# Performance work log

Hardware: AMD Instinct MI355X
Metric: run time of the kernel (lower is better)

## Reference

```python
import jax, jax.numpy as jnp
import numpy as np

N = 100000      # nodes
E = 3200000     # edges
D_IN, D_H, D_OUT = 128, 64, 32


def _lin(key, fan_in, fan_out):
    kw, kb = jax.random.split(key)
    s = 1.0 / np.sqrt(fan_in)
    W = jax.random.uniform(kw, (fan_in, fan_out), jnp.float32, -s, s)
    b = jax.random.uniform(kb, (fan_out,), jnp.float32, -s, s)
    return W, b


def setup_inputs() -> dict:
    key = jax.random.key(0)
    ks = jax.random.split(key, 8)
    x = jax.random.normal(ks[0], (N, D_IN), jnp.float32)
    edge_index = jax.random.randint(ks[1], (2, E), 0, N, dtype=jnp.int32).astype(jnp.int64)
    W1, b1 = _lin(ks[2], D_IN, D_H)      # GCNConv(128, 64)
    W2, b2 = _lin(ks[3], D_H, D_OUT)     # GCNConv(64, 32)
    rW1, rb1 = _lin(ks[4], D_OUT, D_H)   # reconstruction MLP
    rW2, rb2 = _lin(ks[5], D_H, D_IN)
    sW1, sb1 = _lin(ks[6], D_OUT, D_H // 2)  # anomaly scorer MLP
    sW2, sb2 = _lin(ks[7], D_H // 2, 1)
    return {"x": x, "edge_index": edge_index,
            "W1": W1, "b1": b1, "W2": W2, "b2": b2,
            "rW1": rW1, "rb1": rb1, "rW2": rW2, "rb2": rb2,
            "sW1": sW1, "sb1": sb1, "sW2": sW2, "sb2": sb2}


def gcn_conv(h, W, b, src, dst, deg_inv_sqrt):
    # GCNConv with added self-loops and symmetric normalization.
    hw = h @ W                                   # [N, out]
    norm = deg_inv_sqrt[src] * deg_inv_sqrt[dst] # [E]
    agg = jax.ops.segment_sum(hw[src] * norm[:, None], dst, num_segments=N)
    agg = agg + hw * (deg_inv_sqrt * deg_inv_sqrt)[:, None]  # self-loop term
    return agg + b


def reference(x, edge_index, W1, b1, W2, b2, rW1, rb1, rW2, rb2, sW1, sb1, sW2, sb2):
    src, dst = edge_index[0], edge_index[1]
    # degree with self-loops (in-degree on target, as in PyG gcn_norm)
    deg = jnp.zeros((N,), x.dtype).at[dst].add(1.0) + 1.0
    dis = jax.lax.rsqrt(deg)
    h = gcn_conv(x, W1, b1, src, dst, dis)
    h = jax.nn.relu(h)                           # relu+dropout(eval=no-op) between convs
    h = gcn_conv(h, W2, b2, src, dst, dis)       # [N, 32]
    x_rec = jax.nn.relu(h @ rW1 + rb1) @ rW2 + rb2           # [N, 128]
    score = jax.nn.sigmoid(jax.nn.relu(h @ sW1 + sb1) @ sW2 + sb2)  # [N, 1]
    return h, x_rec, score
```

## Files before the change

kernel.cpp:

```cpp
#include <hip/hip_runtime.h>
#include <hip/hip_bf16.h>
#include <math.h>


__global__ __launch_bounds__(256) void k_binhist(const void* __restrict__ ei,
                                                 int E, int CS, int B, int shift,
                                                 int ndet,
                                                 int* __restrict__ hist, int C) {
  __shared__ int lh[256];
  __shared__ int s32;
  int t = threadIdx.x;
  if (t == 0) s32 = 0;
  for (int i = t; i < B; i += 256) lh[i] = 0;
  __syncthreads();
  {
    const unsigned* w = (const unsigned*)ei;
    int local = 0;
    for (int i = t; i < ndet; i += 256) local |= (w[2 * i + 1] != 0u);
    if (local) atomicOr(&s32, 1);
  }
  __syncthreads();
  bool is64 = (s32 == 0);
  int c = blockIdx.x;
  int e0 = c * CS, e1 = min(E, e0 + CS);
  for (int e = e0 + t; e < e1; e += 256) {
    int d = is64 ? (int)((const long long*)ei)[(long)E + e]
                 : ((const int*)ei)[(long)E + e];
    atomicAdd(&lh[d >> shift], 1);
  }
  __syncthreads();
  for (int b = t; b < B; b += 256) hist[(long)b * C + c] = lh[b];
}

__global__ __launch_bounds__(256) void k_binscatter(const void* __restrict__ ei,
                                                    int E, int CS, int B, int shift,
                                                    int SB, int ndet,
                                                    const int* __restrict__ scan,
                                                    int C, unsigned* __restrict__ pairs) {
  __shared__ int cur[256];
  __shared__ int s32;
  int t = threadIdx.x;
  if (t == 0) s32 = 0;
  int c = blockIdx.x;
  for (int b = t; b < B; b += 256) cur[b] = scan[(long)b * C + c];
  __syncthreads();
  {
    const unsigned* w = (const unsigned*)ei;
    int local = 0;
    for (int i = t; i < ndet; i += 256) local |= (w[2 * i + 1] != 0u);
    if (local) atomicOr(&s32, 1);
  }
  __syncthreads();
  bool is64 = (s32 == 0);
  int e0 = c * CS, e1 = min(E, e0 + CS);
  unsigned spb1 = (1u << shift) - 1u;
  for (int e = e0 + t; e < e1; e += 256) {
    int s, d;
    if (is64) {
      const long long* p = (const long long*)ei;
      s = (int)p[e]; d = (int)p[(long)E + e];
    } else {
      const int* p = (const int*)ei;
      s = p[e]; d = p[(long)E + e];
    }
    int pos = atomicAdd(&cur[d >> shift], 1);
    pairs[pos] = (((unsigned)d & spb1) << SB) | (unsigned)s;
  }
}

#define BB_CAP 16896
__global__ __launch_bounds__(256) void k_bucketbuild(const unsigned* __restrict__ pairs,
                                                     const int* __restrict__ scan,
                                                     int C, int shift, int SB, int N,
                                                     int* __restrict__ cnt,
                                                     float* __restrict__ dis,
                                                     int* __restrict__ rs,
                                                     int* __restrict__ csr) {
  __shared__ unsigned buf[BB_CAP];
  __shared__ unsigned buf2[BB_CAP];
  __shared__ int h[1024];
  __shared__ int sm[256];
  __shared__ int sh[512];
  int bin = blockIdx.x;
  int base = bin << shift;
  int nn = min(N - base, 1 << shift);
  int t = threadIdx.x;
  unsigned smask = (1u << SB) - 1u;
  int p0 = scan[(long)bin * C];
  int p1 = scan[(long)(bin + 1) * C];
  int ne = p1 - p0;
  bool srt = (ne <= BB_CAP);

  if (srt)
    for (int i = t; i < ne; i += 256) buf[i] = pairs[p0 + i];
  for (int i = t; i < 1024; i += 256) h[i] = 0;
  __syncthreads();

  for (int i = t; i < ne; i += 256)
    atomicAdd(&h[(srt ? buf[i] : pairs[p0 + i]) >> SB], 1);
  __syncthreads();

  int v0 = h[4 * t], v1 = h[4 * t + 1], v2 = h[4 * t + 2], v3 = h[4 * t + 3];
  int s = v0 + v1 + v2 + v3;
  sm[t] = s;
  __syncthreads();
  for (int off = 1; off < 256; off <<= 1) {
    int x = (t >= off) ? sm[t - off] : 0;
    __syncthreads();
    sm[t] += x;
    __syncthreads();
  }
  int run = p0 + sm[t] - s;
  int r0 = run, r1 = run + v0, r2 = r1 + v1, r3 = r2 + v2;
  h[4 * t] = r0; h[4 * t + 1] = r1; h[4 * t + 2] = r2; h[4 * t + 3] = r3;
  if (4 * t + 0 < nn) { cnt[base + 4*t+0] = v0; dis[base + 4*t+0] = rsqrtf((float)v0 + 1.f); rs[base + 4*t+0] = r0; }
  if (4 * t + 1 < nn) { cnt[base + 4*t+1] = v1; dis[base + 4*t+1] = rsqrtf((float)v1 + 1.f); rs[base + 4*t+1] = r1; }
  if (4 * t + 2 < nn) { cnt[base + 4*t+2] = v2; dis[base + 4*t+2] = rsqrtf((float)v2 + 1.f); rs[base + 4*t+2] = r2; }
  if (4 * t + 3 < nn) { cnt[base + 4*t+3] = v3; dis[base + 4*t+3] = rsqrtf((float)v3 + 1.f); rs[base + 4*t+3] = r3; }
  __syncthreads();

  if (srt) {
    for (int i = t; i < 512; i += 256) sh[i] = 0;
    __syncthreads();
    for (int i = t; i < ne; i += 256)
      atomicAdd(&sh[(buf[i] & smask) >> 8], 1);
    __syncthreads();
    int a0 = sh[2 * t], a1 = sh[2 * t + 1];
    int ss = a0 + a1;
    sm[t] = ss;
    __syncthreads();
    for (int off = 1; off < 256; off <<= 1) {
      int x = (t >= off) ? sm[t - off] : 0;
      __syncthreads();
      sm[t] += x;
      __syncthreads();
    }
    int rn = sm[t] - ss;
    sh[2 * t] = rn; sh[2 * t + 1] = rn + a0;
    __syncthreads();
    for (int i = t; i < ne; i += 256) {
      unsigned p = buf[i];
      int pos = atomicAdd(&sh[(p & smask) >> 8], 1);
      buf2[pos] = p;
    }
    __syncthreads();
    for (int i = t; i < ne; i += 256) {
      unsigned p = buf2[i];
      int pos = atomicAdd(&h[p >> SB], 1);
      csr[pos] = (int)(p & smask);
    }
  } else {
    for (int i = p0 + t; i < p1; i += 256) {
      unsigned p = pairs[i];
      int pos = atomicAdd(&h[p >> SB], 1);
      csr[pos] = (int)(p & smask);
    }
  }
}

__global__ __launch_bounds__(1024) void k_scan1(const int* __restrict__ cnt,
                                                int* __restrict__ bsums, int n) {
  __shared__ int sm[1024];
  int t = threadIdx.x;
  long i = (long)blockIdx.x * 1024 + t;
  sm[t] = (i < n) ? cnt[i] : 0;
  __syncthreads();
  for (int s = 512; s > 0; s >>= 1) {
    if (t < s) sm[t] += sm[t + s];
    __syncthreads();
  }
  if (t == 0) bsums[blockIdx.x] = sm[0];
}

__global__ void k_scan2(int* __restrict__ bsums, int nb) {
  __shared__ int sm[128];
  int t = threadIdx.x;
  int v = (t < nb) ? bsums[t] : 0;
  sm[t] = v;
  __syncthreads();
  for (int off = 1; off < 128; off <<= 1) {
    int x = (t >= off) ? sm[t - off] : 0;
    __syncthreads();
    sm[t] += x;
    __syncthreads();
  }
  if (t < nb) bsums[t] = sm[t] - v;
}

__global__ __launch_bounds__(1024) void k_scan3s(const int* __restrict__ in,
                                                 const int* __restrict__ bsums,
                                                 int* __restrict__ out, int n,
                                                 int sentinel) {
  __shared__ int sm[1024];
  int t = threadIdx.x;
  long i = (long)blockIdx.x * 1024 + t;
  int v = (i < n) ? in[i] : 0;
  sm[t] = v;
  __syncthreads();
  for (int off = 1; off < 1024; off <<= 1) {
    int x = (t >= off) ? sm[t - off] : 0;
    __syncthreads();
    sm[t] += x;
    __syncthreads();
  }
  int excl = sm[t] - v + bsums[blockIdx.x];
  if (i < n) out[i] = excl;
  if (sentinel && i == n - 1) out[n] = excl + v;
}

__device__ __forceinline__ float bfu(unsigned short u) {
  return __uint_as_float((unsigned)u << 16);
}
__device__ __forceinline__ float bf_lo(unsigned u) {
  return __uint_as_float(u << 16);
}
__device__ __forceinline__ float bf_hi(unsigned u) {
  return __uint_as_float(u & 0xffff0000u);
}
__device__ __forceinline__ unsigned pack_bf2(float lo, float hi) {
  __hip_bfloat16 a = __float2bfloat16(lo), b = __float2bfloat16(hi);
  return (unsigned)*(unsigned short*)&a | ((unsigned)*(unsigned short*)&b << 16);
}

template <int K, int M, bool BIAS, int ACT, bool ABF16, bool OBF16>
__global__ __launch_bounds__(256) void k_gemm(const void* __restrict__ Av,
                                              const float* __restrict__ W,
                                              const float* __restrict__ bias,
                                              void* __restrict__ Cout, int nrows) {
  constexpr int CP = 4;
  constexpr int TPR = M / CP;
  constexpr int RG = 256 / TPR;
  constexpr int RP = 4;
  constexpr int RT = RG * RP;
  __shared__ __align__(16) float sW[K * M];
  __shared__ __align__(16) float sB[BIAS ? M : 4];

  for (int i = threadIdx.x; i < K * M / 4; i += 256)
    ((float4*)sW)[i] = ((const float4*)W)[i];
  if (BIAS)
    for (int i = threadIdx.x; i < M; i += 256) sB[i] = bias[i];
  __syncthreads();

  const int cg = threadIdx.x % TPR;
  const int rg = threadIdx.x / TPR;
  const long row0 = (long)blockIdx.x * RT + rg;

  const float4* Apf[RP];
  const ushort4* Apb[RP];
  bool valid[RP];
#pragma unroll
  for (int r = 0; r < RP; ++r) {
    long row = row0 + (long)r * RG;
    valid[r] = (row < nrows);
    long rr = valid[r] ? row : 0;
    if (ABF16) Apb[r] = (const ushort4*)((const unsigned short*)Av + rr * K);
    else       Apf[r] = (const float4*)((const float*)Av + rr * K);
  }

  auto loadA = [&](int r, int k4) -> float4 {
    if (!valid[r]) return make_float4(0.f, 0.f, 0.f, 0.f);
    if (ABF16) {
      ushort4 q = Apb[r][k4];
      return make_float4(bfu(q.x), bfu(q.y), bfu(q.z), bfu(q.w));
    }
    return Apf[r][k4];
  };

  float acc[RP][CP] = {};
  float4 a[RP];
#pragma unroll
  for (int r = 0; r < RP; ++r) a[r] = loadA(r, 0);

#pragma unroll 1
  for (int k0 = 0; k0 < K - 4; k0 += 4) {
    float4 an[RP];
#pragma unroll
    for (int r = 0; r < RP; ++r) an[r] = loadA(r, k0 / 4 + 1);
#pragma unroll
    for (int j = 0; j < 4; ++j) {
      float4 w = ((const float4*)(sW + (k0 + j) * M))[cg];
#pragma unroll
      for (int r = 0; r < RP; ++r) {
        float av = (j == 0) ? a[r].x : (j == 1) ? a[r].y : (j == 2) ? a[r].z : a[r].w;
        acc[r][0] += av * w.x;
        acc[r][1] += av * w.y;
        acc[r][2] += av * w.z;
        acc[r][3] += av * w.w;
      }
    }
#pragma unroll
    for (int r = 0; r < RP; ++r) a[r] = an[r];
  }
  {
    const int k0 = K - 4;
#pragma unroll
    for (int j = 0; j < 4; ++j) {
      float4 w = ((const float4*)(sW + (k0 + j) * M))[cg];
#pragma unroll
      for (int r = 0; r < RP; ++r) {
        float av = (j == 0) ? a[r].x : (j == 1) ? a[r].y : (j == 2) ? a[r].z : a[r].w;
        acc[r][0] += av * w.x;
        acc[r][1] += av * w.y;
        acc[r][2] += av * w.z;
        acc[r][3] += av * w.w;
      }
    }
  }

#pragma unroll
  for (int r = 0; r < RP; ++r) {
    long row = row0 + (long)r * RG;
    if (row >= nrows) continue;
    float4 o = make_float4(acc[r][0], acc[r][1], acc[r][2], acc[r][3]);
    if (BIAS) {
      float4 bb = ((const float4*)sB)[cg];
      o.x += bb.x; o.y += bb.y; o.z += bb.z; o.w += bb.w;
    }
    if (ACT == 1) {
      o.x = fmaxf(o.x, 0.f); o.y = fmaxf(o.y, 0.f);
      o.z = fmaxf(o.z, 0.f); o.w = fmaxf(o.w, 0.f);
    }
    if (OBF16) {
      uint2 pk;
      pk.x = pack_bf2(o.x, o.y);
      pk.y = pack_bf2(o.z, o.w);
      ((uint2*)((__hip_bfloat16*)Cout + row * M))[cg] = pk;
    } else {
      ((float4*)((float*)Cout + row * M))[cg] = o;
    }
  }
}

__global__ __launch_bounds__(256) void k_agg64g(const uint2* __restrict__ hw,
                                                const int* __restrict__ csr,
                                                const int* __restrict__ rs,
                                                const int* __restrict__ cnt,
                                                const float* __restrict__ dis,
                                                const float* __restrict__ b,
                                                const float* __restrict__ W2,
                                                unsigned* __restrict__ hw2,
                                                int n) {
  __shared__ __align__(16) float sW2[64 * 32];
  __shared__ __align__(16) float sH[16][68];
  int t = threadIdx.x;
  for (int i = t; i < 64 * 32 / 4; i += 256)
    ((float4*)sW2)[i] = ((const float4*)W2)[i];

  unsigned nd = t >> 4;
  unsigned node = blockIdx.x * 16u + nd;
  unsigned f4 = t & 15;
  bool ok = (node < (unsigned)n);
  float o0 = 0.f, o1 = 0.f, o2 = 0.f, o3 = 0.f;
  if (ok) {
    float dsn = dis[node];
    uint2 su = hw[node * 16u + f4];
    float d2 = dsn * dsn;
    float a0 = bf_lo(su.x) * d2, a1 = bf_hi(su.x) * d2;
    float a2 = bf_lo(su.y) * d2, a3 = bf_hi(su.y) * d2;
    int start = rs[node], deg = cnt[node];
    int e = 0;
    for (; e + 7 < deg; e += 8) {
      unsigned s0 = (unsigned)csr[start + e];
      unsigned s1 = (unsigned)csr[start + e + 1];
      unsigned s2 = (unsigned)csr[start + e + 2];
      unsigned s3 = (unsigned)csr[start + e + 3];
      unsigned s4 = (unsigned)csr[start + e + 4];
      unsigned s5 = (unsigned)csr[start + e + 5];
      unsigned s6 = (unsigned)csr[start + e + 6];
      unsigned s7 = (unsigned)csr[start + e + 7];
      float w0 = dis[s0] * dsn, w1 = dis[s1] * dsn;
      float w2 = dis[s2] * dsn, w3 = dis[s3] * dsn;
      float w4 = dis[s4] * dsn, w5 = dis[s5] * dsn;
      float w6 = dis[s6] * dsn, w7 = dis[s7] * dsn;
      uint2 u0 = hw[s0 * 16u + f4];
      uint2 u1 = hw[s1 * 16u + f4];
      uint2 u2 = hw[s2 * 16u + f4];
      uint2 u3 = hw[s3 * 16u + f4];
      uint2 u4 = hw[s4 * 16u + f4];
      uint2 u5 = hw[s5 * 16u + f4];
      uint2 u6 = hw[s6 * 16u + f4];
      uint2 u7 = hw[s7 * 16u + f4];
      a0 += bf_lo(u0.x) * w0 + bf_lo(u1.x) * w1 + bf_lo(u2.x) * w2 + bf_lo(u3.x) * w3
          + bf_lo(u4.x) * w4 + bf_lo(u5.x) * w5 + bf_lo(u6.x) * w6 + bf_lo(u7.x) * w7;
      a1 += bf_hi(u0.x) * w0 + bf_hi(u1.x) * w1 + bf_hi(u2.x) * w2 + bf_hi(u3.x) * w3
          + bf_hi(u4.x) * w4 + bf_hi(u5.x) * w5 + bf_hi(u6.x) * w6 + bf_hi(u7.x) * w7;
      a2 += bf_lo(u0.y) * w0 + bf_lo(u1.y) * w1 + bf_lo(u2.y) * w2 + bf_lo(u3.y) * w3
          + bf_lo(u4.y) * w4 + bf_lo(u5.y) * w5 + bf_lo(u6.y) * w6 + bf_lo(u7.y) * w7;
      a3 += bf_hi(u0.y) * w0 + bf_hi(u1.y) * w1 + bf_hi(u2.y) * w2 + bf_hi(u3.y) * w3
          + bf_hi(u4.y) * w4 + bf_hi(u5.y) * w5 + bf_hi(u6.y) * w6 + bf_hi(u7.y) * w7;
    }
    for (; e < deg; ++e) {
      unsigned s0 = (unsigned)csr[start + e];
      float w0 = dis[s0] * dsn;
      uint2 u0 = hw[s0 * 16u + f4];
      a0 += bf_lo(u0.x) * w0;
      a1 += bf_hi(u0.x) * w0;
      a2 += bf_lo(u0.y) * w0;
      a3 += bf_hi(u0.y) * w0;
    }
    float4 bb = ((const float4*)b)[f4];
    o0 = fmaxf(a0 + bb.x, 0.f);
    o1 = fmaxf(a1 + bb.y, 0.f);
    o2 = fmaxf(a2 + bb.z, 0.f);
    o3 = fmaxf(a3 + bb.w, 0.f);
  }
  ((float4*)&sH[nd][4 * f4])[0] = make_float4(o0, o1, o2, o3);
  __syncthreads();
  if (ok) {
    float acc0 = 0.f, acc1 = 0.f;
#pragma unroll 8
    for (int k = 0; k < 64; ++k) {
      float hv = sH[nd][k];
      float2 w = *(const float2*)(sW2 + k * 32 + 2 * f4);
      acc0 += hv * w.x;
      acc1 += hv * w.y;
    }
    hw2[node * 16u + f4] = pack_bf2(acc0, acc1);
  }
}

__global__ __launch_bounds__(256) void k_agg32p(const uint2* __restrict__ hw,
                                                const int* __restrict__ csr,
                                                const int* __restrict__ rs,
                                                const int* __restrict__ cnt,
                                                const float* __restrict__ dis,
                                                const float* __restrict__ b,
                                                float* __restrict__ out, int n) {
  unsigned node = blockIdx.x * 32u + (threadIdx.x >> 3);
  if (node >= (unsigned)n) return;
  unsigned f4 = threadIdx.x & 7;
  float dsn = dis[node];
  uint2 su = hw[node * 8u + f4];
  float d2 = dsn * dsn;
  float a0 = bf_lo(su.x) * d2, a1 = bf_hi(su.x) * d2;
  float a2 = bf_lo(su.y) * d2, a3 = bf_hi(su.y) * d2;
  int start = rs[node], deg = cnt[node];
  int e = 0;
  for (; e + 7 < deg; e += 8) {
    unsigned s0 = (unsigned)csr[start + e];
    unsigned s1 = (unsigned)csr[start + e + 1];
    unsigned s2 = (unsigned)csr[start + e + 2];
    unsigned s3 = (unsigned)csr[start + e + 3];
    unsigned s4 = (unsigned)csr[start + e + 4];
    unsigned s5 = (unsigned)csr[start + e + 5];
    unsigned s6 = (unsigned)csr[start + e + 6];
    unsigned s7 = (unsigned)csr[start + e + 7];
    float w0 = dis[s0] * dsn, w1 = dis[s1] * dsn;
    float w2 = dis[s2] * dsn, w3 = dis[s3] * dsn;
    float w4 = dis[s4] * dsn, w5 = dis[s5] * dsn;
    float w6 = dis[s6] * dsn, w7 = dis[s7] * dsn;
    uint2 u0 = hw[s0 * 8u + f4];
    uint2 u1 = hw[s1 * 8u + f4];
    uint2 u2 = hw[s2 * 8u + f4];
    uint2 u3 = hw[s3 * 8u + f4];
    uint2 u4 = hw[s4 * 8u + f4];
    uint2 u5 = hw[s5 * 8u + f4];
    uint2 u6 = hw[s6 * 8u + f4];
    uint2 u7 = hw[s7 * 8u + f4];
    a0 += bf_lo(u0.x) * w0 + bf_lo(u1.x) * w1 + bf_lo(u2.x) * w2 + bf_lo(u3.x) * w3
        + bf_lo(u4.x) * w4 + bf_lo(u5.x) * w5 + bf_lo(u6.x) * w6 + bf_lo(u7.x) * w7;
    a1 += bf_hi(u0.x) * w0 + bf_hi(u1.x) * w1 + bf_hi(u2.x) * w2 + bf_hi(u3.x) * w3
        + bf_hi(u4.x) * w4 + bf_hi(u5.x) * w5 + bf_hi(u6.x) * w6 + bf_hi(u7.x) * w7;
    a2 += bf_lo(u0.y) * w0 + bf_lo(u1.y) * w1 + bf_lo(u2.y) * w2 + bf_lo(u3.y) * w3
        + bf_lo(u4.y) * w4 + bf_lo(u5.y) * w5 + bf_lo(u6.y) * w6 + bf_lo(u7.y) * w7;
    a3 += bf_hi(u0.y) * w0 + bf_hi(u1.y) * w1 + bf_hi(u2.y) * w2 + bf_hi(u3.y) * w3
        + bf_hi(u4.y) * w4 + bf_hi(u5.y) * w5 + bf_hi(u6.y) * w6 + bf_hi(u7.y) * w7;
  }
  for (; e < deg; ++e) {
    unsigned s0 = (unsigned)csr[start + e];
    float w0 = dis[s0] * dsn;
    uint2 u0 = hw[s0 * 8u + f4];
    a0 += bf_lo(u0.x) * w0;
    a1 += bf_hi(u0.x) * w0;
    a2 += bf_lo(u0.y) * w0;
    a3 += bf_hi(u0.y) * w0;
  }
  float4 bb = ((const float4*)b)[f4];
  ((float4*)(out + node * 32u))[f4] =
      make_float4(a0 + bb.x, a1 + bb.y, a2 + bb.z, a3 + bb.w);
}

__global__ __launch_bounds__(256) void k_tail(const float* __restrict__ h,
                                              const float* __restrict__ rW1,
                                              const float* __restrict__ rb1,
                                              const float* __restrict__ rW2,
                                              const float* __restrict__ rb2,
                                              const float* __restrict__ sW1,
                                              const float* __restrict__ sb1,
                                              const float* __restrict__ sW2,
                                              const float* __restrict__ sb2,
                                              float* __restrict__ x_rec,
                                              float* __restrict__ score, int n) {
  __shared__ __align__(16) float sRW1[32 * 64];
  __shared__ __align__(16) float sRW2[64 * 128];
  __shared__ __align__(16) float sSW1[32 * 32];
  __shared__ __align__(16) float sRB1[64];
  __shared__ __align__(16) float sRB2[128];
  __shared__ __align__(16) float sSB1[32];
  __shared__ __align__(16) float sSW2[32];
  __shared__ float sH[64 * 33];
  __shared__ float sT[64 * 65];
  __shared__ float sS[64 * 33];
  int t = threadIdx.x;
  for (int i = t; i < 32 * 64 / 4; i += 256) ((float4*)sRW1)[i] = ((const float4*)rW1)[i];
  for (int i = t; i < 64 * 128 / 4; i += 256) ((float4*)sRW2)[i] = ((const float4*)rW2)[i];
  for (int i = t; i < 32 * 32 / 4; i += 256) ((float4*)sSW1)[i] = ((const float4*)sW1)[i];
  if (t < 64) sRB1[t] = rb1[t];
  else if (t < 192) sRB2[t - 64] = rb2[t - 64];
  else if (t < 224) sSB1[t - 192] = sb1[t - 192];
  else sSW2[t - 224] = sW2[t - 224];

  long base = (long)blockIdx.x * 64;
  int nn = (int)min(64L, (long)n - base);
  if (nn < 0) nn = 0;
  for (int i = t; i < 64 * 8; i += 256) {
    int node = i >> 3, q = i & 7;
    float4 v = (node < nn) ? ((const float4*)(h + (base + node) * 32))[q]
                           : make_float4(0.f, 0.f, 0.f, 0.f);
    sH[node * 33 + 4 * q]     = v.x;
    sH[node * 33 + 4 * q + 1] = v.y;
    sH[node * 33 + 4 * q + 2] = v.z;
    sH[node * 33 + 4 * q + 3] = v.w;
  }
  __syncthreads();

  {
    int cg = t & 15, rg = t >> 4;
    float acc[4][4] = {};
    for (int k = 0; k < 32; ++k) {
      float4 w = ((const float4*)(sRW1 + k * 64))[cg];
      float a0 = sH[rg * 33 + k];
      float a1 = sH[(rg + 16) * 33 + k];
      float a2 = sH[(rg + 32) * 33 + k];
      float a3 = sH[(rg + 48) * 33 + k];
      acc[0][0] += a0 * w.x; acc[0][1] += a0 * w.y; acc[0][2] += a0 * w.z; acc[0][3] += a0 * w.w;
      acc[1][0] += a1 * w.x; acc[1][1] += a1 * w.y; acc[1][2] += a1 * w.z; acc[1][3] += a1 * w.w;
      acc[2][0] += a2 * w.x; acc[2][1] += a2 * w.y; acc[2][2] += a2 * w.z; acc[2][3] += a2 * w.w;
      acc[3][0] += a3 * w.x; acc[3][1] += a3 * w.y; acc[3][2] += a3 * w.z; acc[3][3] += a3 * w.w;
    }
    float4 bb = ((const float4*)sRB1)[cg];
#pragma unroll
    for (int m = 0; m < 4; ++m) {
      int row = rg + 16 * m;
      sT[row * 65 + 4 * cg]     = fmaxf(acc[m][0] + bb.x, 0.f);
      sT[row * 65 + 4 * cg + 1] = fmaxf(acc[m][1] + bb.y, 0.f);
      sT[row * 65 + 4 * cg + 2] = fmaxf(acc[m][2] + bb.z, 0.f);
      sT[row * 65 + 4 * cg + 3] = fmaxf(acc[m][3] + bb.w, 0.f);
    }
  }
  {
    int cg = t & 7, rg = t >> 3;
    float acc[2][4] = {};
    for (int k = 0; k < 32; ++k) {
      float4 w = ((const float4*)(sSW1 + k * 32))[cg];
      float a0 = sH[rg * 33 + k];
      float a1 = sH[(rg + 32) * 33 + k];
      acc[0][0] += a0 * w.x; acc[0][1] += a0 * w.y; acc[0][2] += a0 * w.z; acc[0][3] += a0 * w.w;
      acc[1][0] += a1 * w.x; acc[1][1] += a1 * w.y; acc[1][2] += a1 * w.z; acc[1][3] += a1 * w.w;
    }
    float4 bb = ((const float4*)sSB1)[cg];
#pragma unroll
    for (int m = 0; m < 2; ++m) {
      int row = rg + 32 * m;
      sS[row * 33 + 4 * cg]     = fmaxf(acc[m][0] + bb.x, 0.f);
      sS[row * 33 + 4 * cg + 1] = fmaxf(acc[m][1] + bb.y, 0.f);
      sS[row * 33 + 4 * cg + 2] = fmaxf(acc[m][2] + bb.z, 0.f);
      sS[row * 33 + 4 * cg + 3] = fmaxf(acc[m][3] + bb.w, 0.f);
    }
  }
  __syncthreads();

  {
    int cg = t & 31, rg = t >> 5;
    float acc[8][4] = {};
    for (int k = 0; k < 64; ++k) {
      float4 w = ((const float4*)(sRW2 + k * 128))[cg];
#pragma unroll
      for (int m = 0; m < 8; ++m) {
        float a = sT[(rg + 8 * m) * 65 + k];
        acc[m][0] += a * w.x; acc[m][1] += a * w.y;
        acc[m][2] += a * w.z; acc[m][3] += a * w.w;
      }
    }
    float4 bb = ((const float4*)sRB2)[cg];
#pragma unroll
    for (int m = 0; m < 8; ++m) {
      int row = rg + 8 * m;
      if (row < nn) {
        float4 o = make_float4(acc[m][0] + bb.x, acc[m][1] + bb.y,
                               acc[m][2] + bb.z, acc[m][3] + bb.w);
        ((float4*)(x_rec + (base + row) * 128))[cg] = o;
      }
    }
  }
  if (t < nn) {
    float acc = 0.f;
    for (int j = 0; j < 32; ++j) acc += sS[t * 33 + j] * sSW2[j];
    score[base + t] = 1.0f / (1.0f + expf(-(acc + sb2[0])));
  }
}

extern "C" void kernel_launch(void* const* d_in, const int* in_sizes, int n_in,
                              void* d_out, int out_size, void* d_ws, size_t ws_size,
                              hipStream_t stream) {
  const float* x   = (const float*)d_in[0];
  const void*  ei  = d_in[1];
  const float* W1  = (const float*)d_in[2];
  const float* b1  = (const float*)d_in[3];
  const float* W2  = (const float*)d_in[4];
  const float* b2  = (const float*)d_in[5];
  const float* rW1 = (const float*)d_in[6];
  const float* rb1 = (const float*)d_in[7];
  const float* rW2 = (const float*)d_in[8];
  const float* rb2 = (const float*)d_in[9];
  const float* sW1 = (const float*)d_in[10];
  const float* sb1 = (const float*)d_in[11];
  const float* sW2 = (const float*)d_in[12];
  const float* sb2 = (const float*)d_in[13];

  const int N = in_sizes[0] / 128;
  const int E = in_sizes[1] / 2;
  const int ndet = E < 4096 ? E : 4096;

  int shift = 9;
  while ((((long)N + (1L << shift) - 1) >> shift) > 256) ++shift;
  const int SB = 32 - shift;
  const int B = (int)(((long)N + (1L << shift) - 1) >> shift);
  const int C = 512;
  const int CS = (E + C - 1) / C;
  const int L = B * C;

  char* w = (char*)d_ws;
  auto alloc = [&](size_t bytes) {
    char* p = w;
    w += (bytes + 255) & ~(size_t)255;
    return p;
  };
  int*   cnt    = (int*)alloc((size_t)N * 4);
  int*   rs     = (int*)alloc((size_t)N * 4);
  float* dis    = (float*)alloc((size_t)N * 4);
  int*   bsumsL = (int*)alloc(1024);
  int*   bscan  = (int*)alloc(((size_t)L + 1) * 4);
  int*   csr    = (int*)alloc((size_t)E * 4);
  unsigned* pairs = (unsigned*)alloc((size_t)E * 4);
  uint2* hw1 = (uint2*)alloc((size_t)N * 64 * 2);
  unsigned* hw2 = (unsigned*)alloc((size_t)N * 32 * 2);

  float* h_out = (float*)d_out;
  float* x_rec = h_out + (long)N * 32;
  float* score = x_rec + (long)N * 128;

  k_binhist<<<C, 256, 0, stream>>>(ei, E, CS, B, shift, ndet, bscan, C);
  int nbL = (L + 1023) / 1024;
  k_scan1<<<nbL, 1024, 0, stream>>>(bscan, bsumsL, L);
  k_scan2<<<1, 128, 0, stream>>>(bsumsL, nbL);
  k_scan3s<<<nbL, 1024, 0, stream>>>(bscan, bsumsL, bscan, L, 1);
  k_binscatter<<<C, 256, 0, stream>>>(ei, E, CS, B, shift, SB, ndet, bscan, C, pairs);
  k_bucketbuild<<<B, 256, 0, stream>>>(pairs, bscan, C, shift, SB, N, cnt, dis, rs, csr);

  k_gemm<128, 64, false, 0, false, true><<<(N + 63) / 64, 256, 0, stream>>>(x, W1, nullptr, hw1, N);
  k_agg64g<<<(N + 15) / 16, 256, 0, stream>>>(hw1, csr, rs, cnt, dis, b1, W2, hw2, N);

  k_agg32p<<<(N + 31) / 32, 256, 0, stream>>>((const uint2*)hw2, csr, rs, cnt, dis, b2, h_out, N);

  k_tail<<<(N + 63) / 64, 256, 0, stream>>>(h_out, rW1, rb1, rW2, rb2,
                                            sW1, sb1, sW2, sb2, x_rec, score, N);
}
```

Before: 281.1 us.

## Fuse second-layer aggregation with reconstruction and scorer MLP tail

Merges the layer-2 aggregation kernel and the MLP tail kernel into one kernel. Each block aggregates 32 nodes, keeps the resulting h in shared memory and runs both MLPs on it directly, so h is no longer re-read from global memory and one launch is removed. The 32KB shared copy of rW2 is dropped and that weight is read straight from global/L1, shrinking shared memory per block. In exchange every block reloads the tail weights for only 32 nodes, and the MLP phase waits on the slowest node's gather in each block.

Result: faster. 264.4 us, median of 2 (-5.9%).

```diff
diff --git a/kernel.cpp b/kernel.cpp
--- a/kernel.cpp
+++ b/kernel.cpp
@@ -419,128 +419,119 @@
   }
 }
 
-__global__ __launch_bounds__(256) void k_agg32p(const uint2* __restrict__ hw,
-                                                const int* __restrict__ csr,
-                                                const int* __restrict__ rs,
-                                                const int* __restrict__ cnt,
-                                                const float* __restrict__ dis,
-                                                const float* __restrict__ b,
-                                                float* __restrict__ out, int n) {
-  unsigned node = blockIdx.x * 32u + (threadIdx.x >> 3);
-  if (node >= (unsigned)n) return;
-  unsigned f4 = threadIdx.x & 7;
-  float dsn = dis[node];
-  uint2 su = hw[node * 8u + f4];
-  float d2 = dsn * dsn;
-  float a0 = bf_lo(su.x) * d2, a1 = bf_hi(su.x) * d2;
-  float a2 = bf_lo(su.y) * d2, a3 = bf_hi(su.y) * d2;
-  int start = rs[node], deg = cnt[node];
-  int e = 0;
-  for (; e + 7 < deg; e += 8) {
-    unsigned s0 = (unsigned)csr[start + e];
-    unsigned s1 = (unsigned)csr[start + e + 1];
-    unsigned s2 = (unsigned)csr[start + e + 2];
-    unsigned s3 = (unsigned)csr[start + e + 3];
-    unsigned s4 = (unsigned)csr[start + e + 4];
-    unsigned s5 = (unsigned)csr[start + e + 5];
-    unsigned s6 = (unsigned)csr[start + e + 6];
-    unsigned s7 = (unsigned)csr[start + e + 7];
-    float w0 = dis[s0] * dsn, w1 = dis[s1] * dsn;
-    float w2 = dis[s2] * dsn, w3 = dis[s3] * dsn;
-    float w4 = dis[s4] * dsn, w5 = dis[s5] * dsn;
-    float w6 = dis[s6] * dsn, w7 = dis[s7] * dsn;
-    uint2 u0 = hw[s0 * 8u + f4];
-    uint2 u1 = hw[s1 * 8u + f4];
-    uint2 u2 = hw[s2 * 8u + f4];
-    uint2 u3 = hw[s3 * 8u + f4];
-    uint2 u4 = hw[s4 * 8u + f4];
-    uint2 u5 = hw[s5 * 8u + f4];
-    uint2 u6 = hw[s6 * 8u + f4];
-    uint2 u7 = hw[s7 * 8u + f4];
-    a0 += bf_lo(u0.x) * w0 + bf_lo(u1.x) * w1 + bf_lo(u2.x) * w2 + bf_lo(u3.x) * w3
-        + bf_lo(u4.x) * w4 + bf_lo(u5.x) * w5 + bf_lo(u6.x) * w6 + bf_lo(u7.x) * w7;
-    a1 += bf_hi(u0.x) * w0 + bf_hi(u1.x) * w1 + bf_hi(u2.x) * w2 + bf_hi(u3.x) * w3
-        + bf_hi(u4.x) * w4 + bf_hi(u5.x) * w5 + bf_hi(u6.x) * w6 + bf_hi(u7.x) * w7;
-    a2 += bf_lo(u0.y) * w0 + bf_lo(u1.y) * w1 + bf_lo(u2.y) * w2 + bf_lo(u3.y) * w3
-        + bf_lo(u4.y) * w4 + bf_lo(u5.y) * w5 + bf_lo(u6.y) * w6 + bf_lo(u7.y) * w7;
-    a3 += bf_hi(u0.y) * w0 + bf_hi(u1.y) * w1 + bf_hi(u2.y) * w2 + bf_hi(u3.y) * w3
-        + bf_hi(u4.y) * w4 + bf_hi(u5.y) * w5 + bf_hi(u6.y) * w6 + bf_hi(u7.y) * w7;
-  }
-  for (; e < deg; ++e) {
-    unsigned s0 = (unsigned)csr[start + e];
-    float w0 = dis[s0] * dsn;
-    uint2 u0 = hw[s0 * 8u + f4];
-    a0 += bf_lo(u0.x) * w0;
-    a1 += bf_hi(u0.x) * w0;
-    a2 += bf_lo(u0.y) * w0;
-    a3 += bf_hi(u0.y) * w0;
-  }
-  float4 bb = ((const float4*)b)[f4];
-  ((float4*)(out + node * 32u))[f4] =
-      make_float4(a0 + bb.x, a1 + bb.y, a2 + bb.z, a3 + bb.w);
-}
-
-__global__ __launch_bounds__(256) void k_tail(const float* __restrict__ h,
-                                              const float* __restrict__ rW1,
-                                              const float* __restrict__ rb1,
-                                              const float* __restrict__ rW2,
-                                              const float* __restrict__ rb2,
-                                              const float* __restrict__ sW1,
-                                              const float* __restrict__ sb1,
-                                              const float* __restrict__ sW2,
-                                              const float* __restrict__ sb2,
-                                              float* __restrict__ x_rec,
-                                              float* __restrict__ score, int n) {
+__global__ __launch_bounds__(256) void k_aggtail(const uint2* __restrict__ hw,
+                                                 const int* __restrict__ csr,
+                                                 const int* __restrict__ rs,
+                                                 const int* __restrict__ cnt,
+                                                 const float* __restrict__ dis,
+                                                 const float* __restrict__ b2,
+                                                 const float* __restrict__ rW1,
+                                                 const float* __restrict__ rb1,
+                                                 const float* __restrict__ rW2,
+                                                 const float* __restrict__ rb2,
+                                                 const float* __restrict__ sW1,
+                                                 const float* __restrict__ sb1,
+                                                 const float* __restrict__ sW2,
+                                                 const float* __restrict__ sb2,
+                                                 float* __restrict__ h_out,
+                                                 float* __restrict__ x_rec,
+                                                 float* __restrict__ score, int n) {
   __shared__ __align__(16) float sRW1[32 * 64];
-  __shared__ __align__(16) float sRW2[64 * 128];
   __shared__ __align__(16) float sSW1[32 * 32];
   __shared__ __align__(16) float sRB1[64];
   __shared__ __align__(16) float sRB2[128];
   __shared__ __align__(16) float sSB1[32];
   __shared__ __align__(16) float sSW2[32];
-  __shared__ float sH[64 * 33];
-  __shared__ float sT[64 * 65];
-  __shared__ float sS[64 * 33];
+  __shared__ float sH[32 * 33];
+  __shared__ float sT[32 * 65];
+  __shared__ float sS[32 * 33];
   int t = threadIdx.x;
   for (int i = t; i < 32 * 64 / 4; i += 256) ((float4*)sRW1)[i] = ((const float4*)rW1)[i];
-  for (int i = t; i < 64 * 128 / 4; i += 256) ((float4*)sRW2)[i] = ((const float4*)rW2)[i];
   for (int i = t; i < 32 * 32 / 4; i += 256) ((float4*)sSW1)[i] = ((const float4*)sW1)[i];
   if (t < 64) sRB1[t] = rb1[t];
   else if (t < 192) sRB2[t - 64] = rb2[t - 64];
   else if (t < 224) sSB1[t - 192] = sb1[t - 192];
   else sSW2[t - 224] = sW2[t - 224];
 
-  long base = (long)blockIdx.x * 64;
-  int nn = (int)min(64L, (long)n - base);
+  unsigned ndl = t >> 3;
+  unsigned node = blockIdx.x * 32u + ndl;
+  unsigned f4 = t & 7;
+  bool ok = (node < (unsigned)n);
+  float o0 = 0.f, o1 = 0.f, o2 = 0.f, o3 = 0.f;
+  if (ok) {
+    float dsn = dis[node];
+    uint2 su = hw[node * 8u + f4];
+    float d2 = dsn * dsn;
+    float a0 = bf_lo(su.x) * d2, a1 = bf_hi(su.x) * d2;
+    float a2 = bf_lo(su.y) * d2, a3 = bf_hi(su.y) * d2;
+    int start = rs[node], deg = cnt[node];
+    int e = 0;
+    for (; e + 7 < deg; e += 8) {
+      unsigned s0 = (unsigned)csr[start + e];
+      unsigned s1 = (unsigned)csr[start + e + 1];
+      unsigned s2 = (unsigned)csr[start + e + 2];
+      unsigned s3 = (unsigned)csr[start + e + 3];
+      unsigned s4 = (unsigned)csr[start + e + 4];
+      unsigned s5 = (unsigned)csr[start + e + 5];
+      unsigned s6 = (unsigned)csr[start + e + 6];
+      unsigned s7 = (unsigned)csr[start + e + 7];
+      float w0 = dis[s0] * dsn, w1 = dis[s1] * dsn;
+      float w2 = dis[s2] * dsn, w3 = dis[s3] * dsn;
+      float w4 = dis[s4] * dsn, w5 = dis[s5] * dsn;
+      float w6 = dis[s6] * dsn, w7 = dis[s7] * dsn;
+      uint2 u0 = hw[s0 * 8u + f4];
+      uint2 u1 = hw[s1 * 8u + f4];
+      uint2 u2 = hw[s2 * 8u + f4];
+      uint2 u3 = hw[s3 * 8u + f4];
+      uint2 u4 = hw[s4 * 8u + f4];
+      uint2 u5 = hw[s5 * 8u + f4];
+      uint2 u6 = hw[s6 * 8u + f4];
+      uint2 u7 = hw[s7 * 8u + f4];
+      a0 += bf_lo(u0.x) * w0 + bf_lo(u1.x) * w1 + bf_lo(u2.x) * w2 + bf_lo(u3.x) * w3
+          + bf_lo(u4.x) * w4 + bf_lo(u5.x) * w5 + bf_lo(u6.x) * w6 + bf_lo(u7.x) * w7;
+      a1 += bf_hi(u0.x) * w0 + bf_hi(u1.x) * w1 + bf_hi(u2.x) * w2 + bf_hi(u3.x) * w3
+          + bf_hi(u4.x) * w4 + bf_hi(u5.x) * w5 + bf_hi(u6.x) * w6 + bf_hi(u7.x) * w7;
+      a2 += bf_lo(u0.y) * w0 + bf_lo(u1.y) * w1 + bf_lo(u2.y) * w2 + bf_lo(u3.y) * w3
+          + bf_lo(u4.y) * w4 + bf_lo(u5.y) * w5 + bf_lo(u6.y) * w6 + bf_lo(u7.y) * w7;
+      a3 += bf_hi(u0.y) * w0 + bf_hi(u1.y) * w1 + bf_hi(u2.y) * w2 + bf_hi(u3.y) * w3
+          + bf_hi(u4.y) * w4 + bf_hi(u5.y) * w5 + bf_hi(u6.y) * w6 + bf_hi(u7.y) * w7;
+    }
+    for (; e < deg; ++e) {
+      unsigned s0 = (unsigned)csr[start + e];
+      float w0 = dis[s0] * dsn;
+      uint2 u0 = hw[s0 * 8u + f4];
+      a0 += bf_lo(u0.x) * w0;
+      a1 += bf_hi(u0.x) * w0;
+      a2 += bf_lo(u0.y) * w0;
+      a3 += bf_hi(u0.y) * w0;
+    }
+    float4 bb = ((const float4*)b2)[f4];
+    o0 = a0 + bb.x; o1 = a1 + bb.y; o2 = a2 + bb.z; o3 = a3 + bb.w;
+    ((float4*)(h_out + node * 32u))[f4] = make_float4(o0, o1, o2, o3);
+  }
+  sH[ndl * 33 + 4 * f4]     = o0;
+  sH[ndl * 33 + 4 * f4 + 1] = o1;
+  sH[ndl * 33 + 4 * f4 + 2] = o2;
+  sH[ndl * 33 + 4 * f4 + 3] = o3;
+  __syncthreads();
+
+  long base = (long)blockIdx.x * 32;
+  int nn = (int)min(32L, (long)n - base);
   if (nn < 0) nn = 0;
-  for (int i = t; i < 64 * 8; i += 256) {
-    int node = i >> 3, q = i & 7;
-    float4 v = (node < nn) ? ((const float4*)(h + (base + node) * 32))[q]
-                           : make_float4(0.f, 0.f, 0.f, 0.f);
-    sH[node * 33 + 4 * q]     = v.x;
-    sH[node * 33 + 4 * q + 1] = v.y;
-    sH[node * 33 + 4 * q + 2] = v.z;
-    sH[node * 33 + 4 * q + 3] = v.w;
-  }
-  __syncthreads();
 
   {
     int cg = t & 15, rg = t >> 4;
-    float acc[4][4] = {};
+    float acc[2][4] = {};
     for (int k = 0; k < 32; ++k) {
       float4 w = ((const float4*)(sRW1 + k * 64))[cg];
       float a0 = sH[rg * 33 + k];
       float a1 = sH[(rg + 16) * 33 + k];
-      float a2 = sH[(rg + 32) * 33 + k];
-      float a3 = sH[(rg + 48) * 33 + k];
       acc[0][0] += a0 * w.x; acc[0][1] += a0 * w.y; acc[0][2] += a0 * w.z; acc[0][3] += a0 * w.w;
       acc[1][0] += a1 * w.x; acc[1][1] += a1 * w.y; acc[1][2] += a1 * w.z; acc[1][3] += a1 * w.w;
-      acc[2][0] += a2 * w.x; acc[2][1] += a2 * w.y; acc[2][2] += a2 * w.z; acc[2][3] += a2 * w.w;
-      acc[3][0] += a3 * w.x; acc[3][1] += a3 * w.y; acc[3][2] += a3 * w.z; acc[3][3] += a3 * w.w;
     }
     float4 bb = ((const float4*)sRB1)[cg];
 #pragma unroll
-    for (int m = 0; m < 4; ++m) {
+    for (int m = 0; m < 2; ++m) {
       int row = rg + 16 * m;
       sT[row * 65 + 4 * cg]     = fmaxf(acc[m][0] + bb.x, 0.f);
       sT[row * 65 + 4 * cg + 1] = fmaxf(acc[m][1] + bb.y, 0.f);
@@ -550,33 +541,27 @@
   }
   {
     int cg = t & 7, rg = t >> 3;
-    float acc[2][4] = {};
+    float acc[4] = {};
     for (int k = 0; k < 32; ++k) {
       float4 w = ((const float4*)(sSW1 + k * 32))[cg];
       float a0 = sH[rg * 33 + k];
-      float a1 = sH[(rg + 32) * 33 + k];
-      acc[0][0] += a0 * w.x; acc[0][1] += a0 * w.y; acc[0][2] += a0 * w.z; acc[0][3] += a0 * w.w;
-      acc[1][0] += a1 * w.x; acc[1][1] += a1 * w.y; acc[1][2] += a1 * w.z; acc[1][3] += a1 * w.w;
+      acc[0] += a0 * w.x; acc[1] += a0 * w.y; acc[2] += a0 * w.z; acc[3] += a0 * w.w;
     }
     float4 bb = ((const float4*)sSB1)[cg];
-#pragma unroll
-    for (int m = 0; m < 2; ++m) {
-      int row = rg + 32 * m;
-      sS[row * 33 + 4 * cg]     = fmaxf(acc[m][0] + bb.x, 0.f);
-      sS[row * 33 + 4 * cg + 1] = fmaxf(acc[m][1] + bb.y, 0.f);
-      sS[row * 33 + 4 * cg + 2] = fmaxf(acc[m][2] + bb.z, 0.f);
-      sS[row * 33 + 4 * cg + 3] = fmaxf(acc[m][3] + bb.w, 0.f);
-    }
+    sS[rg * 33 + 4 * cg]     = fmaxf(acc[0] + bb.x, 0.f);
+    sS[rg * 33 + 4 * cg + 1] = fmaxf(acc[1] + bb.y, 0.f);
+    sS[rg * 33 + 4 * cg + 2] = fmaxf(acc[2] + bb.z, 0.f);
+    sS[rg * 33 + 4 * cg + 3] = fmaxf(acc[3] + bb.w, 0.f);
   }
   __syncthreads();
 
   {
     int cg = t & 31, rg = t >> 5;
-    float acc[8][4] = {};
+    float acc[4][4] = {};
     for (int k = 0; k < 64; ++k) {
-      float4 w = ((const float4*)(sRW2 + k * 128))[cg];
-#pragma unroll
-      for (int m = 0; m < 8; ++m) {
+      float4 w = ((const float4*)(rW2 + k * 128))[cg];
+#pragma unroll
+      for (int m = 0; m < 4; ++m) {
         float a = sT[(rg + 8 * m) * 65 + k];
         acc[m][0] += a * w.x; acc[m][1] += a * w.y;
         acc[m][2] += a * w.z; acc[m][3] += a * w.w;
@@ -584,7 +569,7 @@
     }
     float4 bb = ((const float4*)sRB2)[cg];
 #pragma unroll
-    for (int m = 0; m < 8; ++m) {
+    for (int m = 0; m < 4; ++m) {
       int row = rg + 8 * m;
       if (row < nn) {
         float4 o = make_float4(acc[m][0] + bb.x, acc[m][1] + bb.y,
@@ -661,8 +646,7 @@
   k_gemm<128, 64, false, 0, false, true><<<(N + 63) / 64, 256, 0, stream>>>(x, W1, nullptr, hw1, N);
   k_agg64g<<<(N + 15) / 16, 256, 0, stream>>>(hw1, csr, rs, cnt, dis, b1, W2, hw2, N);
 
-  k_agg32p<<<(N + 31) / 32, 256, 0, stream>>>((const uint2*)hw2, csr, rs, cnt, dis, b2, h_out, N);
-
-  k_tail<<<(N + 63) / 64, 256, 0, stream>>>(h_out, rW1, rb1, rW2, rb2,
-                                            sW1, sb1, sW2, sb2, x_rec, score, N);
-}
+  k_aggtail<<<(N + 31) / 32, 256, 0, stream>>>((const uint2*)hw2, csr, rs, cnt, dis, b2,
+                                               rW1, rb1, rW2, rb2, sW1, sb1, sW2, sb2,
+                                               h_out, x_rec, score, N);
+}
```
